# Kernel tuning notes

Measured on AMD Instinct MI355X. Metric: run time of the kernel, lower is better.

Reference implementation:

```python
import jax, jax.numpy as jnp
import numpy as np

BT, N, C, H, W = 1, 4, 64, 28, 60
ZC, YC, XC = 200, 8, 200  # grid dims (Zcam, Ycam, Xcam); voxel_shape=[200,200,8] -> Z=200, X=200, Y=8
OUT_C = 128
EPS = 1e-6


def setup_inputs() -> dict:
    key = jax.random.key(0)
    k1, k2, k3, k4 = jax.random.split(key, 4)
    # normalized sampling coords in ~[-1.2, 1.2] so some points fall outside the image (zero-padded)
    voxcam_coords = jax.random.uniform(k1, (BT, N, ZC, YC, XC, 3), jnp.float32, -1.2, 1.2)
    # binary visibility mask per voxel-camera pair
    vox_valid = (jax.random.uniform(k2, (BT, N, ZC, YC, XC, 1)) < 0.5).astype(jnp.float32)
    img_feats = jax.random.normal(k3, (BT, N, C, H, W), jnp.float32)
    W_comp = jax.random.normal(k4, (OUT_C, C * YC), jnp.float32) * 0.02  # MLP-as-1x1-conv height compressor
    b_comp = jnp.zeros((OUT_C,), jnp.float32)
    return {"voxcam_coords": voxcam_coords, "vox_valid": vox_valid, "img_feats": img_feats,
            "W_comp": W_comp, "b_comp": b_comp}


def _grid_sample_3d(feat, grid):
    """Trilinear grid_sample, align_corners=False, zeros padding.
    feat: (B, C, D, H, W); grid: (B, P, 3) with (x, y, z) in [-1, 1]. Returns (B, C, P)."""
    B, Cc, D, Hh, Ww = feat.shape
    x = ((grid[..., 0] + 1.0) * Ww - 1.0) * 0.5
    y = ((grid[..., 1] + 1.0) * Hh - 1.0) * 0.5
    z = ((grid[..., 2] + 1.0) * D - 1.0) * 0.5
    x0f, y0f, z0f = jnp.floor(x), jnp.floor(y), jnp.floor(z)
    wx, wy, wz = x - x0f, y - y0f, z - z0f
    x0, y0, z0 = x0f.astype(jnp.int32), y0f.astype(jnp.int32), z0f.astype(jnp.int32)

    def sample_one(fb, x0b, y0b, z0b, wxb, wyb, wzb):
        out = jnp.zeros((Cc, x0b.shape[0]), fb.dtype)
        for dz in (0, 1):
            for dy in (0, 1):
                for dx in (0, 1):
                    zi, yi, xi = z0b + dz, y0b + dy, x0b + dx
                    valid = ((zi >= 0) & (zi < D) & (yi >= 0) & (yi < Hh)
                             & (xi >= 0) & (xi < Ww)).astype(fb.dtype)
                    v = fb[:, jnp.clip(zi, 0, D - 1), jnp.clip(yi, 0, Hh - 1), jnp.clip(xi, 0, Ww - 1)]
                    w = ((wxb if dx else 1.0 - wxb) * (wyb if dy else 1.0 - wyb)
                         * (wzb if dz else 1.0 - wzb)) * valid
                    out = out + v * w[None]
        return out

    return jax.vmap(sample_one)(feat, x0, y0, z0, wx, wy, wz)


def reference(voxcam_coords, vox_valid, img_feats, W_comp, b_comp):
    bt, n, zc, yc, xc, _ = voxcam_coords.shape
    c, h, w = img_feats.shape[2], img_feats.shape[3], img_feats.shape[4]
    P = zc * yc * xc
    grid = voxcam_coords.reshape(bt * n, P, 3)
    feat = img_feats.reshape(bt * n, c, 1, h, w)  # N_group=1 depth axis
    sampled = _grid_sample_3d(feat, grid).reshape(bt, n, c, zc, yc, xc)
    mask = jnp.transpose(vox_valid, (0, 1, 5, 2, 3, 4))  # (bt, n, 1, zc, yc, xc)
    vox_feats = sampled * mask                      # get_feats_dense_grid_sample masking
    # reduce_cams: masked mean over cameras (dim=1)
    red = (vox_feats * mask).sum(axis=1) / (mask.sum(axis=1) + EPS)  # (bt, c, zc, yc, xc)
    # height compressor: 'bt c z y x -> bt (c y) z x' then 1x1 conv (MLP)
    comp_in = jnp.transpose(red, (0, 1, 3, 2, 4)).reshape(bt, c * yc, zc, xc)
    out = jnp.einsum('bczx,oc->bozx', comp_in, W_comp) + b_comp[None, :, None, None]
    # _unpack_batch: (b*t, C, Z, X) -> (b, t, C, Z, X) with b=t=1
    return out.reshape(1, bt, out.shape[1], zc, xc)
```

## Files before the change

kernel.cpp:

```cpp
#include <hip/hip_runtime.h>
#include <hip/hip_bf16.h>
#include <hip/hip_fp16.h>

#define N_  4
#define C_  64
#define H_  28
#define W_  60
#define ZC_ 200
#define YC_ 8
#define XC_ 200
#define OUTC_ 128
#define KD_ 512
#define EPS_ 1e-6f
#define ZB 4
#define XB 8
#define NCOL 32

typedef __attribute__((ext_vector_type(8))) short short8;
typedef __attribute__((ext_vector_type(4))) float f32x4;

__device__ __forceinline__ unsigned short f2bf(float f) {
    unsigned int u = __float_as_uint(f);
    u += 0x7FFF + ((u >> 16) & 1);
    return (unsigned short)(u >> 16);
}

__global__ void gsvt_prep(const float* __restrict__ img,
                          const float* __restrict__ Wc,
                          unsigned short* __restrict__ featB,
                          unsigned short* __restrict__ Wb) {
    int tid = blockIdx.x * blockDim.x + threadIdx.x;
    int stride = gridDim.x * blockDim.x;
    const int totF = N_ * H_ * W_ * C_;
    for (int i = tid; i < totF; i += stride) {
        int c  = i & 63;
        int hw = i >> 6;
        int w  = hw % W_;
        int nh = hw / W_;
        int h  = nh % H_;
        int n  = nh / H_;
        featB[i] = f2bf(img[((n * C_ + c) * H_ + h) * W_ + w]);
    }
    const int totW = OUTC_ * KD_;
    for (int i = tid; i < totW; i += stride) {
        int k = i & (KD_ - 1);
        int o = i >> 9;
        int y = k >> 6;
        int c = k & 63;
        Wb[i] = f2bf(Wc[o * KD_ + c * YC_ + y]);
    }
}

__device__ __forceinline__ void accp(float2* n, const uint4 V, const float w) {
    float2 f0, f1, f2, f3;
    f0.x = __uint_as_float(V.x << 16); f0.y = __uint_as_float(V.x & 0xFFFF0000u);
    f1.x = __uint_as_float(V.y << 16); f1.y = __uint_as_float(V.y & 0xFFFF0000u);
    f2.x = __uint_as_float(V.z << 16); f2.y = __uint_as_float(V.z & 0xFFFF0000u);
    f3.x = __uint_as_float(V.w << 16); f3.y = __uint_as_float(V.w & 0xFFFF0000u);
    n[0].x += w * f0.x; n[0].y += w * f0.y;
    n[1].x += w * f1.x; n[1].y += w * f1.y;
    n[2].x += w * f2.x; n[2].y += w * f2.y;
    n[3].x += w * f3.x; n[3].y += w * f3.y;
}

__global__ __launch_bounds__(256, 4) void gsvt_fusedR(
        const float* __restrict__ coords,
        const float* __restrict__ validm,
        const unsigned short* __restrict__ featB,
        const unsigned short* __restrict__ Wb,
        const float* __restrict__ bias,
        float* __restrict__ out)
{
    __shared__ unsigned short redB[64][NCOL][8];

    const int z0 = blockIdx.y * ZB;
    const int x0 = blockIdx.x * XB;
    const int t  = threadIdx.x;
    const int wv = t >> 6;
    const int l  = t & 63;

    const int yp = l >> 3;
    const int xp = l & 7;
    const int zs = z0 + wv;
    const int xg = x0 + xp;

    float gxv[4], gyv[4], gzv[4], mmv[4];
    #pragma unroll
    for (int cam = 0; cam < N_; ++cam) {
        const int cb = ((cam * ZC_ + zs) * YC_ + yp) * XC_ + xg;
        gxv[cam] = coords[cb * 3 + 0];
        gyv[cam] = coords[cb * 3 + 1];
        gzv[cam] = coords[cb * 3 + 2];
        mmv[cam] = validm[cb];
    }
    const float inv = 1.0f / (mmv[0] + mmv[1] + mmv[2] + mmv[3] + EPS_);

    unsigned Tx[4], Ty[4];
    #pragma unroll
    for (int cam = 0; cam < N_; ++cam) {
        const float xf = ((gxv[cam] + 1.0f) * (float)W_ - 1.0f) * 0.5f;
        const float yf = ((gyv[cam] + 1.0f) * (float)H_ - 1.0f) * 0.5f;
        const float zf = gzv[cam] * 0.5f;
        const float x0f = floorf(xf), y0f = floorf(yf), z0f = floorf(zf);
        const float wx = xf - x0f, wy = yf - y0f, wz = zf - z0f;
        const int xi = (int)x0f, yi = (int)y0f, zi = (int)z0f;

        const float zw = (zi == 0) ? (1.f - wz) : ((zi == -1) ? wz : 0.f);
        const float s  = mmv[cam] * zw * inv;

        const float wx0 = (xi >= 0 && xi < W_)         ? (1.f - wx) * s : 0.f;
        const float wx1 = (xi + 1 >= 0 && xi + 1 < W_) ? wx * s         : 0.f;
        const float wy0 = (yi >= 0 && yi < H_)         ? (1.f - wy)     : 0.f;
        const float wy1 = (yi + 1 >= 0 && yi + 1 < H_) ? wy             : 0.f;

        const unsigned q00 = (unsigned)(wy0 * wx0 * 4095.f + 0.5f);
        const unsigned q01 = (unsigned)(wy0 * wx1 * 4095.f + 0.5f);
        const unsigned q10 = (unsigned)(wy1 * wx0 * 4095.f + 0.5f);
        const unsigned q11 = (unsigned)(wy1 * wx1 * 4095.f + 0.5f);

        const int xc0 = min(max(xi, 0), W_ - 1);
        const int xc1 = min(max(xi + 1, 0), W_ - 1);
        const int yc0 = min(max(yi, 0), H_ - 1);
        const int yc1 = min(max(yi + 1, 0), H_ - 1);
        const unsigned pixidx = (unsigned)((cam * H_ + yc0) * W_ + xc0);
        const unsigned fdx = (unsigned)(xc1 - xc0);
        const unsigned fdy = (unsigned)(yc1 - yc0);

        Tx[cam] = q00 | (q01 << 12) | ((q10 & 0xFFu) << 24);
        Ty[cam] = (q10 >> 8) | (q11 << 4) | (pixidx << 16)
                | (fdx << 29) | (fdy << 30);
    }

    const int g     = l >> 3;
    const int lane8 = l & 7;
    const unsigned lb = (unsigned)(lane8 << 4);
    const int col   = wv * 8 + g;
    const char* fb  = (const char*)featB;

    #pragma unroll
    for (int y = 0; y < YC_; ++y) {
        const int idx = (y << 3) | g;

        int ax[4], ay[4];
        #pragma unroll
        for (int cam = 0; cam < N_; ++cam) {
            ax[cam] = __shfl((int)Tx[cam], idx);
            ay[cam] = __shfl((int)Ty[cam], idx);
        }

        unsigned baseA[4], dxoA[4], dyoA[4];
        #pragma unroll
        for (int cam = 0; cam < N_; ++cam) {
            const unsigned B = (unsigned)ay[cam];
            baseA[cam] = (((B >> 16) & 0x1FFFu) << 7) + lb;
            dxoA[cam]  = ((B >> 29) & 1u) << 7;
            dyoA[cam]  = ((B >> 30) & 1u) * (unsigned)(W_ * 128);
        }

        uint4 V[4][4];
        #pragma unroll
        for (int cam = 0; cam < N_; ++cam) {
            V[cam][0] = *(const uint4*)(fb + baseA[cam]);
            V[cam][1] = *(const uint4*)(fb + (baseA[cam] + dxoA[cam]));
            V[cam][2] = *(const uint4*)(fb + (baseA[cam] + dyoA[cam]));
            V[cam][3] = *(const uint4*)(fb + (baseA[cam] + dyoA[cam] + dxoA[cam]));
        }

        float2 num[4] = {{0.f,0.f},{0.f,0.f},{0.f,0.f},{0.f,0.f}};
        #pragma unroll
        for (int cam = 0; cam < N_; ++cam) {
            const unsigned A = (unsigned)ax[cam];
            const unsigned B = (unsigned)ay[cam];
            const float w00 = (float)(A & 0xFFFu)                      * (1.f/4095.f);
            const float w01 = (float)((A >> 12) & 0xFFFu)              * (1.f/4095.f);
            const float w10 = (float)((A >> 24) | ((B & 0xFu) << 8))   * (1.f/4095.f);
            const float w11 = (float)((B >> 4) & 0xFFFu)               * (1.f/4095.f);
            accp(num, V[cam][0], w00);
            accp(num, V[cam][1], w01);
            accp(num, V[cam][2], w10);
            accp(num, V[cam][3], w11);
        }

        unsigned r0, r1, r2, r3;
        asm("v_cvt_pk_bf16_f32 %0, %1, %2" : "=v"(r0) : "v"(num[0].x), "v"(num[0].y));
        asm("v_cvt_pk_bf16_f32 %0, %1, %2" : "=v"(r1) : "v"(num[1].x), "v"(num[1].y));
        asm("v_cvt_pk_bf16_f32 %0, %1, %2" : "=v"(r2) : "v"(num[2].x), "v"(num[2].y));
        asm("v_cvt_pk_bf16_f32 %0, %1, %2" : "=v"(r3) : "v"(num[3].x), "v"(num[3].y));

        const int kb   = y * 8 + lane8;
        const int pcol = (col & 16) | ((col ^ kb) & 15);
        *(uint4*)&redB[kb][pcol][0] = make_uint4(r0, r1, r2, r3);
    }
    __syncthreads();

    const int wave = t >> 6;
    const int lane = t & 63;
    const int q    = lane >> 4;
    const int l16  = lane & 15;

    f32x4 acc00 = {0.f,0.f,0.f,0.f}, acc01 = {0.f,0.f,0.f,0.f};
    f32x4 acc10 = {0.f,0.f,0.f,0.f}, acc11 = {0.f,0.f,0.f,0.f};
    const unsigned short* wbase = Wb + (wave * 32 + l16) * KD_;

    #pragma unroll
    for (int ks = 0; ks < 16; ++ks) {
        const int kb = ks * 4 + q;
        const int xs = l16 ^ (kb & 15);
        const short8 B0 = *(const short8*)&redB[kb][xs][0];
        const short8 B1 = *(const short8*)&redB[kb][16 + xs][0];
        const short8 A0 = *(const short8*)(wbase + ks * 32 + q * 8);
        const short8 A1 = *(const short8*)(wbase + 16 * KD_ + ks * 32 + q * 8);
        acc00 = __builtin_amdgcn_mfma_f32_16x16x32_bf16(A0, B0, acc00, 0, 0, 0);
        acc01 = __builtin_amdgcn_mfma_f32_16x16x32_bf16(A0, B1, acc01, 0, 0, 0);
        acc10 = __builtin_amdgcn_mfma_f32_16x16x32_bf16(A1, B0, acc10, 0, 0, 0);
        acc11 = __builtin_amdgcn_mfma_f32_16x16x32_bf16(A1, B1, acc11, 0, 0, 0);
    }

    #pragma unroll
    for (int ct = 0; ct < 2; ++ct) {
        const int c2  = ct * 16 + l16;
        const int zz  = c2 >> 3;
        const int xl  = c2 & 7;
        const int ob  = (z0 + zz) * XC_ + x0 + xl;
        const f32x4 a0 = ct ? acc01 : acc00;
        const f32x4 a1 = ct ? acc11 : acc10;
        #pragma unroll
        for (int j = 0; j < 4; ++j) {
            const int o0 = wave * 32 + q * 4 + j;
            out[o0 * (ZC_ * XC_) + ob] = a0[j] + bias[o0];
            const int o1 = o0 + 16;
            out[o1 * (ZC_ * XC_) + ob] = a1[j] + bias[o1];
        }
    }
}

extern "C" void kernel_launch(void* const* d_in, const int* in_sizes, int n_in,
                              void* d_out, int out_size, void* d_ws, size_t ws_size,
                              hipStream_t stream) {
    const float* coords = (const float*)d_in[0];
    const float* validm = (const float*)d_in[1];
    const float* img    = (const float*)d_in[2];
    const float* Wc     = (const float*)d_in[3];
    const float* bias   = (const float*)d_in[4];
    float* out = (float*)d_out;

    unsigned short* featB = (unsigned short*)d_ws;
    unsigned short* Wb    = featB + (N_ * H_ * W_ * C_);

    gsvt_prep<<<512, 256, 0, stream>>>(img, Wc, featB, Wb);

    dim3 grid(XC_ / XB, ZC_ / ZB);
    gsvt_fusedR<<<grid, 256, 0, stream>>>(coords, validm, featB, Wb, bias, out);
}
```

Before: 56.73 us.

## Double threads per block, split y rows across waves, skip zero-weight taps

Each block now runs 512 threads in 8 waves. Waves split into two halves of the y range for sampling, and the GEMM is split so each wave computes 16 output channels instead of 32. Bilinear taps for a camera are now skipped when all four quantized weights are zero (masked or out-of-image). This roughly halves the per-thread serial gather and MFMA work and cuts useless loads, at the cost of redundant coordinate loads per half, divergent branches, and possibly lower occupancy with 512-thread blocks.

```diff
diff --git a/kernel.cpp b/kernel.cpp
--- a/kernel.cpp
+++ b/kernel.cpp
@@ -63,7 +63,7 @@
     n[3].x += w * f3.x; n[3].y += w * f3.y;
 }
 
-__global__ __launch_bounds__(256, 4) void gsvt_fusedR(
+__global__ __launch_bounds__(512, 4) void gsvt_fusedW(
         const float* __restrict__ coords,
         const float* __restrict__ validm,
         const unsigned short* __restrict__ featB,
@@ -79,9 +79,12 @@
     const int wv = t >> 6;
     const int l  = t & 63;
 
+    const int zsl = wv & 3;
+    const int yh  = wv >> 2;
+
     const int yp = l >> 3;
     const int xp = l & 7;
-    const int zs = z0 + wv;
+    const int zs = z0 + zsl;
     const int xg = x0 + xp;
 
     float gxv[4], gyv[4], gzv[4], mmv[4];
@@ -134,11 +137,12 @@
     const int g     = l >> 3;
     const int lane8 = l & 7;
     const unsigned lb = (unsigned)(lane8 << 4);
-    const int col   = wv * 8 + g;
+    const int col   = zsl * 8 + g;
     const char* fb  = (const char*)featB;
 
     #pragma unroll
-    for (int y = 0; y < YC_; ++y) {
+    for (int i = 0; i < 4; ++i) {
+        const int y   = yh * 4 + i;
         const int idx = (y << 3) | g;
 
         int ax[4], ay[4];
@@ -148,37 +152,28 @@
             ay[cam] = __shfl((int)Ty[cam], idx);
         }
 
-        unsigned baseA[4], dxoA[4], dyoA[4];
-        #pragma unroll
-        for (int cam = 0; cam < N_; ++cam) {
-            const unsigned B = (unsigned)ay[cam];
-            baseA[cam] = (((B >> 16) & 0x1FFFu) << 7) + lb;
-            dxoA[cam]  = ((B >> 29) & 1u) << 7;
-            dyoA[cam]  = ((B >> 30) & 1u) * (unsigned)(W_ * 128);
-        }
-
-        uint4 V[4][4];
-        #pragma unroll
-        for (int cam = 0; cam < N_; ++cam) {
-            V[cam][0] = *(const uint4*)(fb + baseA[cam]);
-            V[cam][1] = *(const uint4*)(fb + (baseA[cam] + dxoA[cam]));
-            V[cam][2] = *(const uint4*)(fb + (baseA[cam] + dyoA[cam]));
-            V[cam][3] = *(const uint4*)(fb + (baseA[cam] + dyoA[cam] + dxoA[cam]));
-        }
-
         float2 num[4] = {{0.f,0.f},{0.f,0.f},{0.f,0.f},{0.f,0.f}};
         #pragma unroll
         for (int cam = 0; cam < N_; ++cam) {
             const unsigned A = (unsigned)ax[cam];
             const unsigned B = (unsigned)ay[cam];
-            const float w00 = (float)(A & 0xFFFu)                      * (1.f/4095.f);
-            const float w01 = (float)((A >> 12) & 0xFFFu)              * (1.f/4095.f);
-            const float w10 = (float)((A >> 24) | ((B & 0xFu) << 8))   * (1.f/4095.f);
-            const float w11 = (float)((B >> 4) & 0xFFFu)               * (1.f/4095.f);
-            accp(num, V[cam][0], w00);
-            accp(num, V[cam][1], w01);
-            accp(num, V[cam][2], w10);
-            accp(num, V[cam][3], w11);
+            if (A | (B & 0xFFFFu)) {
+                const unsigned base = (((B >> 16) & 0x1FFFu) << 7) + lb;
+                const unsigned dxo  = ((B >> 29) & 1u) << 7;
+                const unsigned dyo  = ((B >> 30) & 1u) * (unsigned)(W_ * 128);
+                const uint4 V0 = *(const uint4*)(fb + base);
+                const uint4 V1 = *(const uint4*)(fb + (base + dxo));
+                const uint4 V2 = *(const uint4*)(fb + (base + dyo));
+                const uint4 V3 = *(const uint4*)(fb + (base + dyo + dxo));
+                const float w00 = (float)(A & 0xFFFu)                    * (1.f/4095.f);
+                const float w01 = (float)((A >> 12) & 0xFFFu)            * (1.f/4095.f);
+                const float w10 = (float)((A >> 24) | ((B & 0xFu) << 8)) * (1.f/4095.f);
+                const float w11 = (float)((B >> 4) & 0xFFFu)             * (1.f/4095.f);
+                accp(num, V0, w00);
+                accp(num, V1, w01);
+                accp(num, V2, w10);
+                accp(num, V3, w11);
+            }
         }
 
         unsigned r0, r1, r2, r3;
@@ -193,27 +188,21 @@
     }
     __syncthreads();
 
-    const int wave = t >> 6;
-    const int lane = t & 63;
-    const int q    = lane >> 4;
-    const int l16  = lane & 15;
-
-    f32x4 acc00 = {0.f,0.f,0.f,0.f}, acc01 = {0.f,0.f,0.f,0.f};
-    f32x4 acc10 = {0.f,0.f,0.f,0.f}, acc11 = {0.f,0.f,0.f,0.f};
-    const unsigned short* wbase = Wb + (wave * 32 + l16) * KD_;
+    const int q    = l >> 4;
+    const int l16  = l & 15;
+
+    f32x4 acc0 = {0.f,0.f,0.f,0.f}, acc1 = {0.f,0.f,0.f,0.f};
+    const unsigned short* wbase = Wb + (wv * 16 + l16) * KD_;
 
     #pragma unroll
     for (int ks = 0; ks < 16; ++ks) {
         const int kb = ks * 4 + q;
         const int xs = l16 ^ (kb & 15);
+        const short8 Af = *(const short8*)(wbase + ks * 32 + q * 8);
         const short8 B0 = *(const short8*)&redB[kb][xs][0];
         const short8 B1 = *(const short8*)&redB[kb][16 + xs][0];
-        const short8 A0 = *(const short8*)(wbase + ks * 32 + q * 8);
-        const short8 A1 = *(const short8*)(wbase + 16 * KD_ + ks * 32 + q * 8);
-        acc00 = __builtin_amdgcn_mfma_f32_16x16x32_bf16(A0, B0, acc00, 0, 0, 0);
-        acc01 = __builtin_amdgcn_mfma_f32_16x16x32_bf16(A0, B1, acc01, 0, 0, 0);
-        acc10 = __builtin_amdgcn_mfma_f32_16x16x32_bf16(A1, B0, acc10, 0, 0, 0);
-        acc11 = __builtin_amdgcn_mfma_f32_16x16x32_bf16(A1, B1, acc11, 0, 0, 0);
+        acc0 = __builtin_amdgcn_mfma_f32_16x16x32_bf16(Af, B0, acc0, 0, 0, 0);
+        acc1 = __builtin_amdgcn_mfma_f32_16x16x32_bf16(Af, B1, acc1, 0, 0, 0);
     }
 
     #pragma unroll
@@ -222,14 +211,11 @@
         const int zz  = c2 >> 3;
         const int xl  = c2 & 7;
         const int ob  = (z0 + zz) * XC_ + x0 + xl;
-        const f32x4 a0 = ct ? acc01 : acc00;
-        const f32x4 a1 = ct ? acc11 : acc10;
+        const f32x4 a = ct ? acc1 : acc0;
         #pragma unroll
         for (int j = 0; j < 4; ++j) {
-            const int o0 = wave * 32 + q * 4 + j;
-            out[o0 * (ZC_ * XC_) + ob] = a0[j] + bias[o0];
-            const int o1 = o0 + 16;
-            out[o1 * (ZC_ * XC_) + ob] = a1[j] + bias[o1];
+            const int o = wv * 16 + q * 4 + j;
+            out[o * (ZC_ * XC_) + ob] = a[j] + bias[o];
         }
     }
 }
@@ -250,5 +236,5 @@
     gsvt_prep<<<512, 256, 0, stream>>>(img, Wc, featB, Wb);
 
     dim3 grid(XC_ / XB, ZC_ / ZB);
-    gsvt_fusedR<<<grid, 256, 0, stream>>>(coords, validm, featB, Wb, bias, out);
-}
+    gsvt_fusedW<<<grid, 512, 0, stream>>>(coords, validm, featB, Wb, bias, out);
+}
```

New measurement: 61.23 us. +7.9%, slower.
